# Kernel tuning notes

Hardware: AMD Instinct MI355X
Metric: run time of the kernel (lower is better)

The kernel has to match this reference:

```python
import jax, jax.numpy as jnp
import numpy as np

ALPHA = 3.0   # self.alpha
TAU = 0.1     # contrastive temperature
K = 8         # configs.k (top-k hyperedges per node)


def _scale(x, w, ehy, enod):
    """One scale of incidence_matrix_learn.
    x: [B, L, D] series tokens; w: [ws, D] word tokens;
    ehy: [H, D] hyperedge embedding table; enod: [N, D] node embedding table, N = L + ws.
    Returns (binary incidence matrix [N, H] float32, scalar contrastive loss).
    """
    B = x.shape[0]
    # concat_all[i]: cat(x.permute(0,2,1), word_expanded) -> [B, D, N]
    we = jnp.broadcast_to(w.T[None], (B,) + w.T.shape)          # [B, D, ws]
    concat = jnp.concatenate([jnp.transpose(x, (0, 2, 1)), we], axis=-1)  # [B, D, N]
    N, H = enod.shape[0], ehy.shape[0]
    # adjacency: softmax(relu(alpha * nodeec @ hyperen.T)) along hyperedge dim
    a = enod @ ehy.T                                            # [N, H]
    adj = jax.nn.softmax(jax.nn.relu(ALPHA * a), axis=-1)
    # top-k mask + threshold > 0.5 -> binary incidence matrix
    k = min(H, K)
    _, idx = jax.lax.top_k(adj, k)                              # [N, k]
    mask = jnp.zeros_like(adj).at[jnp.arange(N)[:, None], idx].set(1.0)
    adj_bin = ((adj * mask) > 0.5).astype(jnp.float32)          # [N, H]
    # positives: nodes sharing any hyperedge (build_pos_indices_from_edge_index),
    # equivalent to (A A^T > 0) with self excluded; dropping all-zero columns is a no-op here
    P = (adj_bin @ adj_bin.T > 0) & ~jnp.eye(N, dtype=bool)     # [N, N]
    cnt = P.sum(axis=1)                                         # positives per node
    # acl_loss_batched, vectorized over batch and nodes
    nodes = jnp.transpose(concat, (0, 2, 1))                    # [B, N, D]
    nrm = nodes / jnp.maximum(jnp.linalg.norm(nodes, axis=-1, keepdims=True), 1e-12)
    sim = jnp.einsum('bnd,bmd->bnm', nrm, nrm) / TAU            # [B, N, N]
    denom = jax.nn.logsumexp(sim, axis=-1)                      # [B, N]
    pos_mean = jnp.einsum('bnm,nm->bn', sim, P.astype(sim.dtype)) / jnp.maximum(cnt, 1)
    valid = cnt > 0                                             # [N]
    loss_sum = jnp.sum(jnp.where(valid[None, :], denom - pos_mean, 0.0))
    vc = B * valid.sum()
    loss = jnp.where(vc > 0, loss_sum / jnp.maximum(vc, 1), 0.0)
    return adj_bin, loss


def setup_inputs() -> dict:
    key = jax.random.key(0)
    ks = jax.random.split(key, 8)
    B, D = 64, 512
    return dict(
        x0=jax.random.normal(ks[0], (B, 512, D), dtype=jnp.float32),
        x1=jax.random.normal(ks[1], (B, 256, D), dtype=jnp.float32),
        word0=jax.random.normal(ks[2], (128, D), dtype=jnp.float32),
        word1=jax.random.normal(ks[3], (128, D), dtype=jnp.float32),
        embhy0=jax.random.normal(ks[4], (128, D), dtype=jnp.float32),
        embhy1=jax.random.normal(ks[5], (64, D), dtype=jnp.float32),
        embnod0=jax.random.normal(ks[6], (640, D), dtype=jnp.float32),
        embnod1=jax.random.normal(ks[7], (384, D), dtype=jnp.float32),
    )


def reference(x0, x1, word0, word1, embhy0, embhy1, embnod0, embnod1):
    a0, l0 = _scale(x0, word0, embhy0, embnod0)
    a1, l1 = _scale(x1, word1, embhy1, embnod1)
    return (a0, a1, l0 + l1)
```

## Files before the change

kernel.cpp:

```cpp
#include <hip/hip_runtime.h>


#define DDIM 512
#define BATCH 64
#define NGID 65536

typedef __attribute__((ext_vector_type(8))) short short8;
typedef __attribute__((ext_vector_type(4))) float f32x4;

__device__ __forceinline__ unsigned short f2bf(float f) {
  unsigned int u = __float_as_uint(f);
  u += 0x7fffu + ((u >> 16) & 1u);
  return (unsigned short)(u >> 16);
}

__device__ __forceinline__ void async16(const void* g, void* l) {
  __builtin_amdgcn_global_load_lds(
      (const __attribute__((address_space(1))) unsigned int*)g,
      (__attribute__((address_space(3))) unsigned int*)l, 16, 0, 0);
}

__global__ __launch_bounds__(256) void prep_kernel(
    const float* __restrict__ enod0, const float* __restrict__ ehy0,
    const float* __restrict__ enod1, const float* __restrict__ ehy1,
    float* __restrict__ adj0, float* __restrict__ adj1,
    int* __restrict__ labels0, int* __restrict__ labels1,
    const float* __restrict__ x0, const float* __restrict__ w0,
    const float* __restrict__ x1, const float* __restrict__ w1,
    unsigned short* __restrict__ nhat0, unsigned short* __restrict__ nhat1,
    float* __restrict__ acc) {
  const int t = threadIdx.x;
  if (blockIdx.x < 1024) {
    if (blockIdx.x == 0 && t == 0) { acc[0] = 0.f; acc[1] = 0.f; }
    const bool s0 = blockIdx.x < 640;
    const int n = s0 ? blockIdx.x : blockIdx.x - 640;
    const int H = s0 ? 128 : 64;
    const float* enod = s0 ? enod0 : enod1;
    const float* ehy = s0 ? ehy0 : ehy1;
    float* out_adj = s0 ? adj0 : adj1;
    int* labels = s0 ? labels0 : labels1;
    __shared__ float erow[DDIM];
    __shared__ float red[128];
    __shared__ int lab;
    if (t < 128) ((float4*)erow)[t] = ((const float4*)(enod + (size_t)n * DDIM))[t];
    if (t == 0) lab = -1;
    __syncthreads();
    float v = 0.f;
    if (t < H) {
      const float4* hr = (const float4*)(ehy + (size_t)t * DDIM);
      float a = 0.f;
      #pragma unroll 8
      for (int d = 0; d < DDIM / 4; ++d) {
        float4 h = hr[d];
        float4 e = ((const float4*)erow)[d];
        a = fmaf(h.x, e.x, a); a = fmaf(h.y, e.y, a);
        a = fmaf(h.z, e.z, a); a = fmaf(h.w, e.w, a);
      }
      v = fmaxf(0.f, 3.0f * a);
    }
    if (t < 128) red[t] = v;
    __syncthreads();
    for (int s = 64; s > 0; s >>= 1) {
      if (t < s) red[t] = fmaxf(red[t], red[t + s]);
      __syncthreads();
    }
    const float mx = red[0];
    __syncthreads();
    const float e = (t < H) ? __expf(v - mx) : 0.f;
    if (t < 128) red[t] = e;
    __syncthreads();
    for (int s = 64; s > 0; s >>= 1) {
      if (t < s) red[t] += red[t + s];
      __syncthreads();
    }
    const float sum = red[0];
    if (t < H) {
      const float adj = e / sum;
      const float bin = (adj > 0.5f) ? 1.0f : 0.0f;
      out_adj[(size_t)n * H + t] = bin;
      if (bin > 0.f) lab = t;
    }
    __syncthreads();
    if (t == 0) labels[n] = lab;
  } else {
    const int wave = t >> 6;
    const int lane = t & 63;
    const int g = (blockIdx.x - 1024) * 4 + wave;
    const bool s0 = g < BATCH * 640;
    const int gg = s0 ? g : g - BATCH * 640;
    const int N = s0 ? 640 : 384;
    const int L = s0 ? 512 : 256;
    const float* x = s0 ? x0 : x1;
    const float* w = s0 ? w0 : w1;
    unsigned short* nhat = s0 ? nhat0 : nhat1;
    const int b = gg / N;
    const int n = gg - b * N;
    const float* src = (n < L) ? (x + ((size_t)b * L + n) * DDIM)
                               : (w + (size_t)(n - L) * DDIM);
    const float4* rowp = (const float4*)src;
    const float4 v0 = rowp[lane];
    const float4 v1 = rowp[lane + 64];
    float ss = v0.x * v0.x + v0.y * v0.y + v0.z * v0.z + v0.w * v0.w +
               v1.x * v1.x + v1.y * v1.y + v1.z * v1.z + v1.w * v1.w;
    #pragma unroll
    for (int off = 32; off > 0; off >>= 1) ss += __shfl_xor(ss, off);
    const float rinv = 1.0f / fmaxf(sqrtf(ss), 1e-12f);
    ushort4 o0, o1;
    o0.x = f2bf(v0.x * rinv); o0.y = f2bf(v0.y * rinv);
    o0.z = f2bf(v0.z * rinv); o0.w = f2bf(v0.w * rinv);
    o1.x = f2bf(v1.x * rinv); o1.y = f2bf(v1.y * rinv);
    o1.z = f2bf(v1.z * rinv); o1.w = f2bf(v1.w * rinv);
    ushort4* op = (ushort4*)(nhat + ((size_t)b * N + n) * DDIM);
    op[lane] = o0;
    op[lane + 64] = o1;
  }
}

__global__ __launch_bounds__(256) void cnt_kernel(
    const int* __restrict__ labels0, int* __restrict__ cnt0,
    const int* __restrict__ labels1, int* __restrict__ cnt1,
    int* __restrict__ valid) {
  const bool s0 = blockIdx.x == 0;
  const int* labels = s0 ? labels0 : labels1;
  int* cnt = s0 ? cnt0 : cnt1;
  int* validcnt = s0 ? valid : valid + 1;
  const int N = s0 ? 640 : 384;
  __shared__ int lab[640];
  __shared__ int hist[128];
  __shared__ int vc;
  const int t = threadIdx.x;
  if (t == 0) vc = 0;
  if (t < 128) hist[t] = 0;
  for (int i = t; i < N; i += 256) lab[i] = labels[i];
  __syncthreads();
  for (int i = t; i < N; i += 256)
    if (lab[i] >= 0) atomicAdd(&hist[lab[i]], 1);
  __syncthreads();
  int lv = 0;
  for (int i = t; i < N; i += 256) {
    const int c = (lab[i] >= 0) ? hist[lab[i]] - 1 : 0;
    cnt[i] = c;
    if (c > 0) ++lv;
  }
  if (lv > 0) atomicAdd(&vc, lv);
  __syncthreads();
  if (t == 0) *validcnt = vc;
}

__global__ __launch_bounds__(128, 2) void lse_kernel(
    const unsigned short* __restrict__ nhat0, const int* __restrict__ labels0,
    const unsigned short* __restrict__ nhat1, const int* __restrict__ labels1,
    float2* __restrict__ sp) {
  __shared__ short8 Bbuf[3][512];
  __shared__ float2 redC[2][64];
  const int tid = threadIdx.x;
  const bool s0 = blockIdx.x < 3520;
  const int i = s0 ? blockIdx.x : blockIdx.x - 3520;
  const int b = i & 63;
  int p = i >> 6;
  const int nt = s0 ? 10 : 6;
  int tu = 0;
  while (p >= nt - tu) { p -= nt - tu; ++tu; }
  const int tv = tu + p;
  const bool diag = (tu == tv);
  const int N = s0 ? 640 : 384;
  const unsigned short* nhat = s0 ? nhat0 : nhat1;
  const int* labels = s0 ? labels0 : labels1;
  const int gbase = s0 ? b * 640 : 40960 + b * 384;

  const int wave = tid >> 6;
  const int lane = tid & 63;
  const int lrow = lane & 15;
  const int lq = lane >> 4;

  const size_t base = (size_t)b * N * DDIM;
  const int rw0 = tu * 64 + wave * 32;
  const unsigned short* Ap0 = nhat + base + (size_t)(rw0 + lrow) * DDIM + lq * 8;
  const unsigned short* Ap1 = Ap0 + (size_t)16 * DDIM;
  short8 a0[16], a1[16];
  #pragma unroll
  for (int ks = 0; ks < 16; ++ks) {
    a0[ks] = *(const short8*)(Ap0 + ks * 32);
    a1[ks] = *(const short8*)(Ap1 + ks * 32);
  }
  int labn[2][4];
  #pragma unroll
  for (int s = 0; s < 2; ++s)
    #pragma unroll
    for (int r = 0; r < 4; ++r) labn[s][r] = labels[rw0 + s * 16 + lq * 4 + r];
  int labm[4];
  #pragma unroll
  for (int j = 0; j < 4; ++j) labm[j] = labels[tv * 64 + j * 16 + lrow];

  __syncthreads();

  const unsigned short* Bp = nhat + base + (size_t)(tv * 64) * DDIM;
  const int f0 = wave * 4;
  #pragma unroll
  for (int pc = 0; pc < 2; ++pc) {
    #pragma unroll
    for (int fi = 0; fi < 4; ++fi) {
      const int f = f0 + fi, j = f >> 1, ks = f & 1;
      async16(Bp + (size_t)(j * 16 + lrow) * DDIM + pc * 64 + ks * 32 + lq * 8,
              &Bbuf[pc][f * 64]);
    }
  }

  f32x4 acc[4][2];
  #pragma unroll
  for (int j = 0; j < 4; ++j) {
    acc[j][0] = (f32x4){0.f, 0.f, 0.f, 0.f};
    acc[j][1] = (f32x4){0.f, 0.f, 0.f, 0.f};
  }
  #pragma unroll
  for (int kc = 0; kc < 8; ++kc) {
    if (kc < 7) asm volatile("s_waitcnt vmcnt(4)" ::: "memory");
    else        asm volatile("s_waitcnt vmcnt(0)" ::: "memory");
    __builtin_amdgcn_s_barrier();
    if (kc < 6) {
      short8* dst = &Bbuf[(kc + 2) % 3][0];
      #pragma unroll
      for (int fi = 0; fi < 4; ++fi) {
        const int f = f0 + fi, j = f >> 1, ks = f & 1;
        async16(Bp + (size_t)(j * 16 + lrow) * DDIM + (kc + 2) * 64 + ks * 32 + lq * 8,
                dst + f * 64);
      }
    }
    const short8* bb = &Bbuf[kc % 3][0];
    #pragma unroll
    for (int ks = 0; ks < 2; ++ks) {
      const short8 b0 = bb[(0 + ks) * 64 + lane];
      const short8 b1 = bb[(2 + ks) * 64 + lane];
      const short8 b2 = bb[(4 + ks) * 64 + lane];
      const short8 b3 = bb[(6 + ks) * 64 + lane];
      const short8 av0 = a0[kc * 2 + ks];
      const short8 av1 = a1[kc * 2 + ks];
      acc[0][0] = __builtin_amdgcn_mfma_f32_16x16x32_bf16(av0, b0, acc[0][0], 0, 0, 0);
      acc[0][1] = __builtin_amdgcn_mfma_f32_16x16x32_bf16(av1, b0, acc[0][1], 0, 0, 0);
      acc[1][0] = __builtin_amdgcn_mfma_f32_16x16x32_bf16(av0, b1, acc[1][0], 0, 0, 0);
      acc[1][1] = __builtin_amdgcn_mfma_f32_16x16x32_bf16(av1, b1, acc[1][1], 0, 0, 0);
      acc[2][0] = __builtin_amdgcn_mfma_f32_16x16x32_bf16(av0, b2, acc[2][0], 0, 0, 0);
      acc[2][1] = __builtin_amdgcn_mfma_f32_16x16x32_bf16(av1, b2, acc[2][1], 0, 0, 0);
      acc[3][0] = __builtin_amdgcn_mfma_f32_16x16x32_bf16(av0, b3, acc[3][0], 0, 0, 0);
      acc[3][1] = __builtin_amdgcn_mfma_f32_16x16x32_bf16(av1, b3, acc[3][1], 0, 0, 0);
    }
  }

  float rSE[2][4] = {{0.f, 0.f, 0.f, 0.f}, {0.f, 0.f, 0.f, 0.f}};
  float rPOS[2][4] = {{0.f, 0.f, 0.f, 0.f}, {0.f, 0.f, 0.f, 0.f}};
  float cSE[4] = {0.f, 0.f, 0.f, 0.f};
  float cPOS[4] = {0.f, 0.f, 0.f, 0.f};
  #pragma unroll
  for (int j = 0; j < 4; ++j) {
    const int v = tv * 64 + j * 16 + lrow;
    #pragma unroll
    for (int s = 0; s < 2; ++s) {
      const int u0 = rw0 + s * 16 + lq * 4;
      #pragma unroll
      for (int r = 0; r < 4; ++r) {
        const float sim = acc[j][s][r] * 10.0f;
        const float e = __expf(sim - 10.0f);
        rSE[s][r] += e;
        const bool match = (labn[s][r] >= 0) && (labm[j] == labn[s][r]);
        if (match && v != u0 + r) rPOS[s][r] += sim;
        if (!diag) {
          cSE[j] += e;
          if (match) cPOS[j] += sim;
        }
      }
    }
  }

  #pragma unroll
  for (int off = 1; off <= 8; off <<= 1) {
    #pragma unroll
    for (int s = 0; s < 2; ++s)
      #pragma unroll
      for (int r = 0; r < 4; ++r) {
        rSE[s][r] += __shfl_xor(rSE[s][r], off);
        rPOS[s][r] += __shfl_xor(rPOS[s][r], off);
      }
  }
  if (lrow == 0) {
    #pragma unroll
    for (int s = 0; s < 2; ++s)
      #pragma unroll
      for (int r = 0; r < 4; ++r) {
        const int u = rw0 + s * 16 + lq * 4 + r;
        float2 st; st.x = rSE[s][r]; st.y = rPOS[s][r];
        sp[(size_t)tv * NGID + gbase + u] = st;
      }
  }

  if (!diag) {
    #pragma unroll
    for (int off = 16; off <= 32; off <<= 1) {
      #pragma unroll
      for (int j = 0; j < 4; ++j) {
        cSE[j] += __shfl_xor(cSE[j], off);
        cPOS[j] += __shfl_xor(cPOS[j], off);
      }
    }
    if (lane < 16) {
      #pragma unroll
      for (int j = 0; j < 4; ++j) {
        float2 st; st.x = cSE[j]; st.y = cPOS[j];
        redC[wave][j * 16 + lane] = st;
      }
    }
    __syncthreads();
    if (tid < 64) {
      const float2 c0 = redC[0][tid];
      const float2 c1 = redC[1][tid];
      const int v = tv * 64 + tid;
      float2 st; st.x = c0.x + c1.x; st.y = c0.y + c1.y;
      sp[(size_t)tu * NGID + gbase + v] = st;
    }
  }
}

__global__ __launch_bounds__(256) void loss_reduce(
    const float2* __restrict__ sp, const int* __restrict__ cnt0,
    const int* __restrict__ cnt1, float* __restrict__ acc) {
  __shared__ float r0[4], r1[4];
  const int t = threadIdx.x;
  float l0 = 0.f, l1 = 0.f;
  for (int g = blockIdx.x * 256 + t; g < NGID; g += 64 * 256) {
    const bool is0 = g < 40960;
    const int nslots = is0 ? 10 : 6;
    float se = 0.f, pos = 0.f;
    for (int s = 0; s < nslots; ++s) {
      const float2 v = sp[(size_t)s * NGID + g];
      se += v.x; pos += v.y;
    }
    const int n = is0 ? (g % 640) : ((g - 40960) % 384);
    const int c = is0 ? cnt0[n] : cnt1[n];
    if (c > 0) {
      const float v = (10.0f + logf(se)) - pos / (float)c;
      if (is0) l0 += v; else l1 += v;
    }
  }
  #pragma unroll
  for (int off = 32; off > 0; off >>= 1) {
    l0 += __shfl_xor(l0, off);
    l1 += __shfl_xor(l1, off);
  }
  if ((t & 63) == 0) { r0[t >> 6] = l0; r1[t >> 6] = l1; }
  __syncthreads();
  if (t == 0) {
    atomicAdd(&acc[0], r0[0] + r0[1] + r0[2] + r0[3]);
    atomicAdd(&acc[1], r1[0] + r1[1] + r1[2] + r1[3]);
  }
}

__global__ void final_kernel(const float* __restrict__ acc,
                             const int* __restrict__ valid,
                             float* __restrict__ out) {
  float l = 0.f;
  if (valid[0] > 0) l += acc[0] / (float)(BATCH * valid[0]);
  if (valid[1] > 0) l += acc[1] / (float)(BATCH * valid[1]);
  out[0] = l;
}

extern "C" void kernel_launch(void* const* d_in, const int* in_sizes, int n_in,
                              void* d_out, int out_size, void* d_ws,
                              size_t ws_size, hipStream_t stream) {
  const float* x0 = (const float*)d_in[0];
  const float* x1 = (const float*)d_in[1];
  const float* w0 = (const float*)d_in[2];
  const float* w1 = (const float*)d_in[3];
  const float* ehy0 = (const float*)d_in[4];
  const float* ehy1 = (const float*)d_in[5];
  const float* enod0 = (const float*)d_in[6];
  const float* enod1 = (const float*)d_in[7];

  float* out = (float*)d_out;
  float* adj0 = out;
  float* adj1 = out + 640 * 128;
  float* lossp = out + 640 * 128 + 384 * 64;

  unsigned short* nhat0 = (unsigned short*)d_ws;
  unsigned short* nhat1 = nhat0 + (size_t)BATCH * 640 * DDIM;
  int* ip = (int*)(nhat1 + (size_t)BATCH * 384 * DDIM);
  int* labels0 = ip;
  int* labels1 = labels0 + 640;
  int* cnt0 = labels1 + 384;
  int* cnt1 = cnt0 + 640;
  int* valid = cnt1 + 384;
  float* acc = (float*)(valid + 2);
  float2* sp = (float2*)((((size_t)(acc + 2)) + 255) & ~(size_t)255);

  prep_kernel<<<1024 + 16384, 256, 0, stream>>>(
      enod0, ehy0, enod1, ehy1, adj0, adj1, labels0, labels1,
      x0, w0, x1, w1, nhat0, nhat1, acc);
  cnt_kernel<<<2, 256, 0, stream>>>(labels0, cnt0, labels1, cnt1, valid);
  lse_kernel<<<4864, 128, 0, stream>>>(nhat0, labels0, nhat1, labels1, sp);
  loss_reduce<<<64, 256, 0, stream>>>(sp, cnt0, cnt1, acc);
  final_kernel<<<1, 1, 0, stream>>>(acc, valid, lossp);
}
```

Baseline: 256.7 us.

## Keep A row-tile resident and loop over column tiles inside one block

The lse kernel now launches one block per (row-tile, batch) and loops over all upper-triangular column tiles, keeping the A fragments in registers and prefetching the next B tile across tile boundaries. This avoids reloading A for every tile pair, and labels are staged in shared memory. The slot layout of partial sums changes: row sums go to slot 0 and column sums to slot 1+tu, so loss_reduce reads only the valid slots. The prep kernel is also split into separate adjacency and normalisation launches. Work per block becomes unbalanced (tile 0 does 10 column tiles, the last does 1), and the grid shrinks from 4864 to 1024 blocks, which may hurt occupancy and tail latency.

```diff
diff --git a/kernel.cpp b/kernel.cpp
--- a/kernel.cpp
+++ b/kernel.cpp
@@ -20,100 +20,107 @@
       (__attribute__((address_space(3))) unsigned int*)l, 16, 0, 0);
 }
 
-__global__ __launch_bounds__(256) void prep_kernel(
+__device__ __forceinline__ int m3(int x) {
+  x -= (x >= 6) ? 6 : 0;
+  x -= (x >= 3) ? 3 : 0;
+  return x;
+}
+
+__global__ __launch_bounds__(256) void prep_adj(
     const float* __restrict__ enod0, const float* __restrict__ ehy0,
     const float* __restrict__ enod1, const float* __restrict__ ehy1,
     float* __restrict__ adj0, float* __restrict__ adj1,
     int* __restrict__ labels0, int* __restrict__ labels1,
+    float* __restrict__ acc) {
+  const int t = threadIdx.x;
+  if (blockIdx.x == 0 && t == 0) { acc[0] = 0.f; acc[1] = 0.f; }
+  const bool s0 = blockIdx.x < 640;
+  const int n = s0 ? blockIdx.x : blockIdx.x - 640;
+  const int H = s0 ? 128 : 64;
+  const float* enod = s0 ? enod0 : enod1;
+  const float* ehy = s0 ? ehy0 : ehy1;
+  float* out_adj = s0 ? adj0 : adj1;
+  int* labels = s0 ? labels0 : labels1;
+  __shared__ float erow[DDIM];
+  __shared__ float red[128];
+  __shared__ int lab;
+  if (t < 128) ((float4*)erow)[t] = ((const float4*)(enod + (size_t)n * DDIM))[t];
+  if (t == 0) lab = -1;
+  __syncthreads();
+  float v = 0.f;
+  if (t < H) {
+    const float4* hr = (const float4*)(ehy + (size_t)t * DDIM);
+    float a = 0.f;
+    #pragma unroll 8
+    for (int d = 0; d < DDIM / 4; ++d) {
+      float4 h = hr[d];
+      float4 e = ((const float4*)erow)[d];
+      a = fmaf(h.x, e.x, a); a = fmaf(h.y, e.y, a);
+      a = fmaf(h.z, e.z, a); a = fmaf(h.w, e.w, a);
+    }
+    v = fmaxf(0.f, 3.0f * a);
+  }
+  if (t < 128) red[t] = v;
+  __syncthreads();
+  for (int s = 64; s > 0; s >>= 1) {
+    if (t < s) red[t] = fmaxf(red[t], red[t + s]);
+    __syncthreads();
+  }
+  const float mx = red[0];
+  __syncthreads();
+  const float e = (t < H) ? __expf(v - mx) : 0.f;
+  if (t < 128) red[t] = e;
+  __syncthreads();
+  for (int s = 64; s > 0; s >>= 1) {
+    if (t < s) red[t] += red[t + s];
+    __syncthreads();
+  }
+  const float sum = red[0];
+  if (t < H) {
+    const float adj = e / sum;
+    const float bin = (adj > 0.5f) ? 1.0f : 0.0f;
+    out_adj[(size_t)n * H + t] = bin;
+    if (bin > 0.f) lab = t;
+  }
+  __syncthreads();
+  if (t == 0) labels[n] = lab;
+}
+
+__global__ __launch_bounds__(256) void prep_norm(
     const float* __restrict__ x0, const float* __restrict__ w0,
     const float* __restrict__ x1, const float* __restrict__ w1,
-    unsigned short* __restrict__ nhat0, unsigned short* __restrict__ nhat1,
-    float* __restrict__ acc) {
+    unsigned short* __restrict__ nhat0, unsigned short* __restrict__ nhat1) {
   const int t = threadIdx.x;
-  if (blockIdx.x < 1024) {
-    if (blockIdx.x == 0 && t == 0) { acc[0] = 0.f; acc[1] = 0.f; }
-    const bool s0 = blockIdx.x < 640;
-    const int n = s0 ? blockIdx.x : blockIdx.x - 640;
-    const int H = s0 ? 128 : 64;
-    const float* enod = s0 ? enod0 : enod1;
-    const float* ehy = s0 ? ehy0 : ehy1;
-    float* out_adj = s0 ? adj0 : adj1;
-    int* labels = s0 ? labels0 : labels1;
-    __shared__ float erow[DDIM];
-    __shared__ float red[128];
-    __shared__ int lab;
-    if (t < 128) ((float4*)erow)[t] = ((const float4*)(enod + (size_t)n * DDIM))[t];
-    if (t == 0) lab = -1;
-    __syncthreads();
-    float v = 0.f;
-    if (t < H) {
-      const float4* hr = (const float4*)(ehy + (size_t)t * DDIM);
-      float a = 0.f;
-      #pragma unroll 8
-      for (int d = 0; d < DDIM / 4; ++d) {
-        float4 h = hr[d];
-        float4 e = ((const float4*)erow)[d];
-        a = fmaf(h.x, e.x, a); a = fmaf(h.y, e.y, a);
-        a = fmaf(h.z, e.z, a); a = fmaf(h.w, e.w, a);
-      }
-      v = fmaxf(0.f, 3.0f * a);
-    }
-    if (t < 128) red[t] = v;
-    __syncthreads();
-    for (int s = 64; s > 0; s >>= 1) {
-      if (t < s) red[t] = fmaxf(red[t], red[t + s]);
-      __syncthreads();
-    }
-    const float mx = red[0];
-    __syncthreads();
-    const float e = (t < H) ? __expf(v - mx) : 0.f;
-    if (t < 128) red[t] = e;
-    __syncthreads();
-    for (int s = 64; s > 0; s >>= 1) {
-      if (t < s) red[t] += red[t + s];
-      __syncthreads();
-    }
-    const float sum = red[0];
-    if (t < H) {
-      const float adj = e / sum;
-      const float bin = (adj > 0.5f) ? 1.0f : 0.0f;
-      out_adj[(size_t)n * H + t] = bin;
-      if (bin > 0.f) lab = t;
-    }
-    __syncthreads();
-    if (t == 0) labels[n] = lab;
-  } else {
-    const int wave = t >> 6;
-    const int lane = t & 63;
-    const int g = (blockIdx.x - 1024) * 4 + wave;
-    const bool s0 = g < BATCH * 640;
-    const int gg = s0 ? g : g - BATCH * 640;
-    const int N = s0 ? 640 : 384;
-    const int L = s0 ? 512 : 256;
-    const float* x = s0 ? x0 : x1;
-    const float* w = s0 ? w0 : w1;
-    unsigned short* nhat = s0 ? nhat0 : nhat1;
-    const int b = gg / N;
-    const int n = gg - b * N;
-    const float* src = (n < L) ? (x + ((size_t)b * L + n) * DDIM)
-                               : (w + (size_t)(n - L) * DDIM);
-    const float4* rowp = (const float4*)src;
-    const float4 v0 = rowp[lane];
-    const float4 v1 = rowp[lane + 64];
-    float ss = v0.x * v0.x + v0.y * v0.y + v0.z * v0.z + v0.w * v0.w +
-               v1.x * v1.x + v1.y * v1.y + v1.z * v1.z + v1.w * v1.w;
-    #pragma unroll
-    for (int off = 32; off > 0; off >>= 1) ss += __shfl_xor(ss, off);
-    const float rinv = 1.0f / fmaxf(sqrtf(ss), 1e-12f);
-    ushort4 o0, o1;
-    o0.x = f2bf(v0.x * rinv); o0.y = f2bf(v0.y * rinv);
-    o0.z = f2bf(v0.z * rinv); o0.w = f2bf(v0.w * rinv);
-    o1.x = f2bf(v1.x * rinv); o1.y = f2bf(v1.y * rinv);
-    o1.z = f2bf(v1.z * rinv); o1.w = f2bf(v1.w * rinv);
-    ushort4* op = (ushort4*)(nhat + ((size_t)b * N + n) * DDIM);
-    op[lane] = o0;
-    op[lane + 64] = o1;
-  }
+  const int wave = t >> 6;
+  const int lane = t & 63;
+  const int g = blockIdx.x * 4 + wave;
+  const bool s0 = g < BATCH * 640;
+  const int gg = s0 ? g : g - BATCH * 640;
+  const int N = s0 ? 640 : 384;
+  const int L = s0 ? 512 : 256;
+  const float* x = s0 ? x0 : x1;
+  const float* w = s0 ? w0 : w1;
+  unsigned short* nhat = s0 ? nhat0 : nhat1;
+  const int b = gg / N;
+  const int n = gg - b * N;
+  const float* src = (n < L) ? (x + ((size_t)b * L + n) * DDIM)
+                             : (w + (size_t)(n - L) * DDIM);
+  const float4* rowp = (const float4*)src;
+  const float4 v0 = rowp[lane];
+  const float4 v1 = rowp[lane + 64];
+  float ss = v0.x * v0.x + v0.y * v0.y + v0.z * v0.z + v0.w * v0.w +
+             v1.x * v1.x + v1.y * v1.y + v1.z * v1.z + v1.w * v1.w;
+  #pragma unroll
+  for (int off = 32; off > 0; off >>= 1) ss += __shfl_xor(ss, off);
+  const float rinv = 1.0f / fmaxf(sqrtf(ss), 1e-12f);
+  ushort4 o0, o1;
+  o0.x = f2bf(v0.x * rinv); o0.y = f2bf(v0.y * rinv);
+  o0.z = f2bf(v0.z * rinv); o0.w = f2bf(v0.w * rinv);
+  o1.x = f2bf(v1.x * rinv); o1.y = f2bf(v1.y * rinv);
+  o1.z = f2bf(v1.z * rinv); o1.w = f2bf(v1.w * rinv);
+  ushort4* op = (ushort4*)(nhat + ((size_t)b * N + n) * DDIM);
+  op[lane] = o0;
+  op[lane + 64] = o1;
 }
 
 __global__ __launch_bounds__(256) void cnt_kernel(
@@ -153,16 +160,13 @@
     float2* __restrict__ sp) {
   __shared__ short8 Bbuf[3][512];
   __shared__ float2 redC[2][64];
+  __shared__ int labS[640];
   const int tid = threadIdx.x;
-  const bool s0 = blockIdx.x < 3520;
-  const int i = s0 ? blockIdx.x : blockIdx.x - 3520;
+  const bool s0 = blockIdx.x < 640;
+  const int i = s0 ? blockIdx.x : blockIdx.x - 640;
+  const int tu = i >> 6;
   const int b = i & 63;
-  int p = i >> 6;
   const int nt = s0 ? 10 : 6;
-  int tu = 0;
-  while (p >= nt - tu) { p -= nt - tu; ++tu; }
-  const int tv = tu + p;
-  const bool diag = (tu == tv);
   const int N = s0 ? 640 : 384;
   const unsigned short* nhat = s0 ? nhat0 : nhat1;
   const int* labels = s0 ? labels0 : labels1;
@@ -172,6 +176,8 @@
   const int lane = tid & 63;
   const int lrow = lane & 15;
   const int lq = lane >> 4;
+
+  for (int t = tid; t < N; t += 128) labS[t] = labels[t];
 
   const size_t base = (size_t)b * N * DDIM;
   const int rw0 = tu * 64 + wave * 32;
@@ -183,92 +189,133 @@
     a0[ks] = *(const short8*)(Ap0 + ks * 32);
     a1[ks] = *(const short8*)(Ap1 + ks * 32);
   }
+  #pragma unroll
+  for (int ks = 0; ks < 16; ++ks)
+    asm volatile("" :: "v"(a0[ks]), "v"(a1[ks]));
+
+  __syncthreads();
+
   int labn[2][4];
   #pragma unroll
   for (int s = 0; s < 2; ++s)
     #pragma unroll
-    for (int r = 0; r < 4; ++r) labn[s][r] = labels[rw0 + s * 16 + lq * 4 + r];
-  int labm[4];
-  #pragma unroll
-  for (int j = 0; j < 4; ++j) labm[j] = labels[tv * 64 + j * 16 + lrow];
-
-  __syncthreads();
-
-  const unsigned short* Bp = nhat + base + (size_t)(tv * 64) * DDIM;
+    for (int r = 0; r < 4; ++r) labn[s][r] = labS[rw0 + s * 16 + lq * 4 + r];
+
+  const unsigned short* Bp0 = nhat + base + (size_t)tu * 64 * DDIM;
   const int f0 = wave * 4;
   #pragma unroll
   for (int pc = 0; pc < 2; ++pc) {
     #pragma unroll
     for (int fi = 0; fi < 4; ++fi) {
       const int f = f0 + fi, j = f >> 1, ks = f & 1;
-      async16(Bp + (size_t)(j * 16 + lrow) * DDIM + pc * 64 + ks * 32 + lq * 8,
+      async16(Bp0 + (size_t)(j * 16 + lrow) * DDIM + pc * 64 + ks * 32 + lq * 8,
               &Bbuf[pc][f * 64]);
-    }
-  }
-
-  f32x4 acc[4][2];
-  #pragma unroll
-  for (int j = 0; j < 4; ++j) {
-    acc[j][0] = (f32x4){0.f, 0.f, 0.f, 0.f};
-    acc[j][1] = (f32x4){0.f, 0.f, 0.f, 0.f};
-  }
-  #pragma unroll
-  for (int kc = 0; kc < 8; ++kc) {
-    if (kc < 7) asm volatile("s_waitcnt vmcnt(4)" ::: "memory");
-    else        asm volatile("s_waitcnt vmcnt(0)" ::: "memory");
-    __builtin_amdgcn_s_barrier();
-    if (kc < 6) {
-      short8* dst = &Bbuf[(kc + 2) % 3][0];
-      #pragma unroll
-      for (int fi = 0; fi < 4; ++fi) {
-        const int f = f0 + fi, j = f >> 1, ks = f & 1;
-        async16(Bp + (size_t)(j * 16 + lrow) * DDIM + (kc + 2) * 64 + ks * 32 + lq * 8,
-                dst + f * 64);
-      }
-    }
-    const short8* bb = &Bbuf[kc % 3][0];
-    #pragma unroll
-    for (int ks = 0; ks < 2; ++ks) {
-      const short8 b0 = bb[(0 + ks) * 64 + lane];
-      const short8 b1 = bb[(2 + ks) * 64 + lane];
-      const short8 b2 = bb[(4 + ks) * 64 + lane];
-      const short8 b3 = bb[(6 + ks) * 64 + lane];
-      const short8 av0 = a0[kc * 2 + ks];
-      const short8 av1 = a1[kc * 2 + ks];
-      acc[0][0] = __builtin_amdgcn_mfma_f32_16x16x32_bf16(av0, b0, acc[0][0], 0, 0, 0);
-      acc[0][1] = __builtin_amdgcn_mfma_f32_16x16x32_bf16(av1, b0, acc[0][1], 0, 0, 0);
-      acc[1][0] = __builtin_amdgcn_mfma_f32_16x16x32_bf16(av0, b1, acc[1][0], 0, 0, 0);
-      acc[1][1] = __builtin_amdgcn_mfma_f32_16x16x32_bf16(av1, b1, acc[1][1], 0, 0, 0);
-      acc[2][0] = __builtin_amdgcn_mfma_f32_16x16x32_bf16(av0, b2, acc[2][0], 0, 0, 0);
-      acc[2][1] = __builtin_amdgcn_mfma_f32_16x16x32_bf16(av1, b2, acc[2][1], 0, 0, 0);
-      acc[3][0] = __builtin_amdgcn_mfma_f32_16x16x32_bf16(av0, b3, acc[3][0], 0, 0, 0);
-      acc[3][1] = __builtin_amdgcn_mfma_f32_16x16x32_bf16(av1, b3, acc[3][1], 0, 0, 0);
     }
   }
 
   float rSE[2][4] = {{0.f, 0.f, 0.f, 0.f}, {0.f, 0.f, 0.f, 0.f}};
   float rPOS[2][4] = {{0.f, 0.f, 0.f, 0.f}, {0.f, 0.f, 0.f, 0.f}};
-  float cSE[4] = {0.f, 0.f, 0.f, 0.f};
-  float cPOS[4] = {0.f, 0.f, 0.f, 0.f};
-  #pragma unroll
-  for (int j = 0; j < 4; ++j) {
-    const int v = tv * 64 + j * 16 + lrow;
-    #pragma unroll
-    for (int s = 0; s < 2; ++s) {
-      const int u0 = rw0 + s * 16 + lq * 4;
+  int slotb = 0;
+
+  for (int tv = tu; tv < nt; ++tv) {
+    const bool diag = (tv == tu);
+    const bool last = (tv == nt - 1);
+    const unsigned short* Bcur = nhat + base + (size_t)tv * 64 * DDIM;
+    const unsigned short* Bnxt = Bcur + (size_t)64 * DDIM;
+    const int sl[3] = {slotb, m3(slotb + 1), m3(slotb + 2)};
+
+    f32x4 acc[4][2];
+    #pragma unroll
+    for (int j = 0; j < 4; ++j) {
+      acc[j][0] = (f32x4){0.f, 0.f, 0.f, 0.f};
+      acc[j][1] = (f32x4){0.f, 0.f, 0.f, 0.f};
+    }
+    #pragma unroll
+    for (int kc = 0; kc < 8; ++kc) {
+      if (last && kc == 7) asm volatile("s_waitcnt vmcnt(0)" ::: "memory");
+      else                 asm volatile("s_waitcnt vmcnt(4)" ::: "memory");
+      __builtin_amdgcn_s_barrier();
+      if (!(last && kc >= 6)) {
+        const unsigned short* Bsrc = (kc < 6) ? Bcur : Bnxt;
+        const int kcol = (kc < 6) ? kc + 2 : kc - 6;
+        short8* dst = &Bbuf[sl[(kc + 2) % 3]][0];
+        #pragma unroll
+        for (int fi = 0; fi < 4; ++fi) {
+          const int f = f0 + fi, j = f >> 1, ks = f & 1;
+          async16(Bsrc + (size_t)(j * 16 + lrow) * DDIM + kcol * 64 + ks * 32 + lq * 8,
+                  dst + f * 64);
+        }
+      }
+      const short8* bb = &Bbuf[sl[kc % 3]][0];
       #pragma unroll
-      for (int r = 0; r < 4; ++r) {
-        const float sim = acc[j][s][r] * 10.0f;
-        const float e = __expf(sim - 10.0f);
-        rSE[s][r] += e;
-        const bool match = (labn[s][r] >= 0) && (labm[j] == labn[s][r]);
-        if (match && v != u0 + r) rPOS[s][r] += sim;
-        if (!diag) {
-          cSE[j] += e;
-          if (match) cPOS[j] += sim;
+      for (int ks = 0; ks < 2; ++ks) {
+        const short8 b0 = bb[(0 + ks) * 64 + lane];
+        const short8 b1 = bb[(2 + ks) * 64 + lane];
+        const short8 b2 = bb[(4 + ks) * 64 + lane];
+        const short8 b3 = bb[(6 + ks) * 64 + lane];
+        const short8 av0 = a0[kc * 2 + ks];
+        const short8 av1 = a1[kc * 2 + ks];
+        acc[0][0] = __builtin_amdgcn_mfma_f32_16x16x32_bf16(av0, b0, acc[0][0], 0, 0, 0);
+        acc[0][1] = __builtin_amdgcn_mfma_f32_16x16x32_bf16(av1, b0, acc[0][1], 0, 0, 0);
+        acc[1][0] = __builtin_amdgcn_mfma_f32_16x16x32_bf16(av0, b1, acc[1][0], 0, 0, 0);
+        acc[1][1] = __builtin_amdgcn_mfma_f32_16x16x32_bf16(av1, b1, acc[1][1], 0, 0, 0);
+        acc[2][0] = __builtin_amdgcn_mfma_f32_16x16x32_bf16(av0, b2, acc[2][0], 0, 0, 0);
+        acc[2][1] = __builtin_amdgcn_mfma_f32_16x16x32_bf16(av1, b2, acc[2][1], 0, 0, 0);
+        acc[3][0] = __builtin_amdgcn_mfma_f32_16x16x32_bf16(av0, b3, acc[3][0], 0, 0, 0);
+        acc[3][1] = __builtin_amdgcn_mfma_f32_16x16x32_bf16(av1, b3, acc[3][1], 0, 0, 0);
+      }
+    }
+
+    float cSE[4] = {0.f, 0.f, 0.f, 0.f};
+    float cPOS[4] = {0.f, 0.f, 0.f, 0.f};
+    #pragma unroll
+    for (int j = 0; j < 4; ++j) {
+      const int v = tv * 64 + j * 16 + lrow;
+      const int labm = labS[v];
+      #pragma unroll
+      for (int s = 0; s < 2; ++s) {
+        const int u0 = rw0 + s * 16 + lq * 4;
+        #pragma unroll
+        for (int r = 0; r < 4; ++r) {
+          const float sim = acc[j][s][r] * 10.0f;
+          const float e = __expf(sim - 10.0f);
+          rSE[s][r] += e;
+          const bool match = (labn[s][r] >= 0) && (labm == labn[s][r]);
+          if (match && v != u0 + r) rPOS[s][r] += sim;
+          if (!diag) {
+            cSE[j] += e;
+            if (match) cPOS[j] += sim;
+          }
         }
       }
     }
+    if (!diag) {
+      #pragma unroll
+      for (int off = 16; off <= 32; off <<= 1) {
+        #pragma unroll
+        for (int j = 0; j < 4; ++j) {
+          cSE[j] += __shfl_xor(cSE[j], off);
+          cPOS[j] += __shfl_xor(cPOS[j], off);
+        }
+      }
+      if (lane < 16) {
+        #pragma unroll
+        for (int j = 0; j < 4; ++j) {
+          float2 st; st.x = cSE[j]; st.y = cPOS[j];
+          redC[wave][j * 16 + lane] = st;
+        }
+      }
+      asm volatile("s_waitcnt lgkmcnt(0)" ::: "memory");
+      __builtin_amdgcn_s_barrier();
+      if (lane < 32) {
+        const int v = wave * 32 + lane;
+        const float2 c0 = redC[0][v];
+        const float2 c1 = redC[1][v];
+        float2 st; st.x = c0.x + c1.x; st.y = c0.y + c1.y;
+        sp[(size_t)(1 + tu) * NGID + gbase + tv * 64 + v] = st;
+      }
+    }
+    slotb = m3(slotb + 2);
   }
 
   #pragma unroll
@@ -288,34 +335,8 @@
       for (int r = 0; r < 4; ++r) {
         const int u = rw0 + s * 16 + lq * 4 + r;
         float2 st; st.x = rSE[s][r]; st.y = rPOS[s][r];
-        sp[(size_t)tv * NGID + gbase + u] = st;
-      }
-  }
-
-  if (!diag) {
-    #pragma unroll
-    for (int off = 16; off <= 32; off <<= 1) {
-      #pragma unroll
-      for (int j = 0; j < 4; ++j) {
-        cSE[j] += __shfl_xor(cSE[j], off);
-        cPOS[j] += __shfl_xor(cPOS[j], off);
-      }
-    }
-    if (lane < 16) {
-      #pragma unroll
-      for (int j = 0; j < 4; ++j) {
-        float2 st; st.x = cSE[j]; st.y = cPOS[j];
-        redC[wave][j * 16 + lane] = st;
-      }
-    }
-    __syncthreads();
-    if (tid < 64) {
-      const float2 c0 = redC[0][tid];
-      const float2 c1 = redC[1][tid];
-      const int v = tv * 64 + tid;
-      float2 st; st.x = c0.x + c1.x; st.y = c0.y + c1.y;
-      sp[(size_t)tu * NGID + gbase + v] = st;
-    }
+        sp[gbase + u] = st;
+      }
   }
 }
 
@@ -327,13 +348,13 @@
   float l0 = 0.f, l1 = 0.f;
   for (int g = blockIdx.x * 256 + t; g < NGID; g += 64 * 256) {
     const bool is0 = g < 40960;
-    const int nslots = is0 ? 10 : 6;
+    const int n = is0 ? (g % 640) : ((g - 40960) % 384);
+    const int tb = n >> 6;
     float se = 0.f, pos = 0.f;
-    for (int s = 0; s < nslots; ++s) {
+    for (int s = 0; s <= tb; ++s) {
       const float2 v = sp[(size_t)s * NGID + g];
       se += v.x; pos += v.y;
     }
-    const int n = is0 ? (g % 640) : ((g - 40960) % 384);
     const int c = is0 ? cnt0[n] : cnt1[n];
     if (c > 0) {
       const float v = (10.0f + logf(se)) - pos / (float)c;
@@ -390,11 +411,11 @@
   float* acc = (float*)(valid + 2);
   float2* sp = (float2*)((((size_t)(acc + 2)) + 255) & ~(size_t)255);
 
-  prep_kernel<<<1024 + 16384, 256, 0, stream>>>(
-      enod0, ehy0, enod1, ehy1, adj0, adj1, labels0, labels1,
-      x0, w0, x1, w1, nhat0, nhat1, acc);
+  prep_adj<<<1024, 256, 0, stream>>>(enod0, ehy0, enod1, ehy1, adj0, adj1,
+                                     labels0, labels1, acc);
+  prep_norm<<<16384, 256, 0, stream>>>(x0, w0, x1, w1, nhat0, nhat1);
   cnt_kernel<<<2, 256, 0, stream>>>(labels0, cnt0, labels1, cnt1, valid);
-  lse_kernel<<<4864, 128, 0, stream>>>(nhat0, labels0, nhat1, labels1, sp);
+  lse_kernel<<<1024, 128, 0, stream>>>(nhat0, labels0, nhat1, labels1, sp);
   loss_reduce<<<64, 256, 0, stream>>>(sp, cnt0, cnt1, acc);
   final_kernel<<<1, 1, 0, stream>>>(acc, valid, lossp);
 }
```

After: 263.0 us. 2.5% more time.
